# Kernel optimization log

Hardware: AMD Instinct MI355X
Metric: run time of the kernel (lower is better)

The kernel has to match this reference:

```python
import jax, jax.numpy as jnp
import numpy as np

# dims: batch, d_features(m), n_subsets, sub_size(k=ceil(m/n)), heads, d_k, d_v, conv kernel, d_out
B, M, N, K, H, DK, DV, KER, D = 512, 4096, 64, 64, 8, 32, 4, 3, 4096
DOUT_PER = D // N  # d_out_per_subset = 64
EPS_LN = 1e-5      # torch nn.LayerNorm default eps


def setup_inputs() -> dict:
    key = jax.random.key(0)
    ks = jax.random.split(key, 8)
    s = 0.02  # xavier-like scale
    return {
        "features": jax.random.normal(ks[0], (B, M), dtype=jnp.float32),
        # per-head permutation of the m feature indices (f_shuffle(m, h, seeds))
        "shuffled_index": jnp.argsort(jax.random.uniform(ks[1], (H, M)), axis=1).astype(jnp.int32),
        "gamma": jnp.ones((M,), jnp.float32),
        "beta": jnp.zeros((M,), jnp.float32),
        "W_q": (jax.random.normal(ks[2], (H * DK, K)) * s).astype(jnp.float32),   # Linear(k, h*d_k)
        "W_k": (jax.random.normal(ks[3], (H, DK, K)) * s).astype(jnp.float32),    # grouped Conv1d(h, h*d_k, kernel=k, stride=k)
        "W_v1": (jax.random.normal(ks[4], (H, DV, KER)) * s).astype(jnp.float32), # grouped Conv1d(h, h*d_v, kernel)
        "W_v2": (jax.random.normal(ks[5], (H, DV)) * s).astype(jnp.float32),      # grouped Conv1d(h*d_v, h, 1)
        "W_fc": (jax.random.normal(ks[6], (DOUT_PER, H * K)) * s).astype(jnp.float32),
    }


def reference(features, shuffled_index, gamma, beta, W_q, W_k, W_v1, W_v2, W_fc):
    b = features.shape[0]
    # LayerNorm over m (query path only)
    mu = features.mean(-1, keepdims=True)
    var = ((features - mu) ** 2).mean(-1, keepdims=True)
    q_in = (features - mu) / jnp.sqrt(var + EPS_LN) * gamma + beta

    # shuffled gather: [b, H, M]  (k*n == m here so k_pad/q_pad are no-ops)
    sf = features[:, shuffled_index]

    # query: [b, n, k] -> Linear(k, h*d_k) -> [b, H, N, DK]
    q = jnp.einsum('bnk,ek->bne', q_in.reshape(b, N, K), W_q)
    q = q.reshape(b, N, H, DK).transpose(0, 2, 1, 3)

    # key: grouped conv kernel=stride=k == per-subset contraction -> [b, H, DK, N]
    kf = sf.reshape(b, H, N, K)
    key_ = jnp.einsum('bhnk,hdk->bhdn', kf, W_k)

    # value: [b, N, H, K], right-pad by KER-1, depthwise conv -> relu -> 1x1 conv -> +residual
    v = kf.transpose(0, 2, 1, 3)  # [b, N, H, K]
    vp = jnp.pad(v, ((0, 0), (0, 0), (0, 0), (0, KER - 1)))
    win = jnp.stack([vp[..., t:t + K] for t in range(KER)], axis=-1)  # [b,N,H,K,KER]
    v1 = jnp.einsum('bnhpt,hdt->bnhdp', win, W_v1)
    v2 = jnp.einsum('bnhdp,hd->bnhp', jax.nn.relu(v1), W_v2)
    v = (v2 + v).transpose(0, 2, 1, 3)  # [b, H, N, K]

    # scaled dot-product attention, temperature = sqrt(m)
    attn = jax.nn.softmax(jnp.einsum('bhqd,bhdk->bhqk', q, key_) / jnp.sqrt(jnp.float32(M)), axis=-1)
    out = jnp.einsum('bhqk,bhks->bhqs', attn, v)           # [b, H, N, K]
    out = out.transpose(0, 2, 1, 3).reshape(b, N, H * K)   # [b, N, H*K]
    out = jnp.einsum('bnf,of->bno', out, W_fc).reshape(b, N * DOUT_PER)
    return out, attn.reshape(b * H, N, N)
```

## Files before the change

### kernel.cpp

```cpp
#include <hip/hip_runtime.h>

typedef __bf16 v8bf __attribute__((ext_vector_type(8)));
typedef __bf16 v4bf __attribute__((ext_vector_type(4)));
typedef __bf16 v2bf __attribute__((ext_vector_type(2)));
typedef float  v4f  __attribute__((ext_vector_type(4)));

namespace {

constexpr int kB = 512, kM = 4096, kH = 8;


__global__ __launch_bounds__(256) void k0_weights(
    const float* __restrict__ Wq, const float* __restrict__ Wk,
    const float* __restrict__ Wfc,
    __bf16* __restrict__ wq, __bf16* __restrict__ wk, __bf16* __restrict__ wfc) {
  int i = blockIdx.x * 256 + threadIdx.x;
  if (i < 16384) {
    int e = i >> 6, k = i & 63;
    int dst = ((e >> 4) * 2 + (k >> 5)) * 512 + (e & 15) * 32 + (k & 31);
    wq[dst] = (__bf16)(Wq[i] * 0.015625f);
  } else if (i < 32768) {
    int j = i - 16384;
    int e = j >> 6, k = j & 63;
    int dst = ((e >> 4) * 2 + (k >> 5)) * 512 + (e & 15) * 32 + (k & 31);
    wk[dst] = (__bf16)Wk[j];
  } else {
    int j = i - 32768;
    int o = j >> 9, f = j & 511;
    int dst = ((o >> 4) * 16 + (f >> 5)) * 512 + (o & 15) * 32 + (f & 31);
    wfc[dst] = (__bf16)Wfc[j];
  }
}

__global__ __launch_bounds__(256, 2) void k_fused(
    const float* __restrict__ feat, const int* __restrict__ sidx,
    const float* __restrict__ gamma, const float* __restrict__ beta,
    const __bf16* __restrict__ wq, const __bf16* __restrict__ wk,
    const float* __restrict__ Wv1, const float* __restrict__ Wv2,
    const __bf16* __restrict__ wfc, float* __restrict__ out) {
  __shared__ __align__(16) __bf16 smem[26624];
  __shared__ float red[4];
  __bf16* s_feat = smem;
  __bf16* s_qin  = smem + 4096;
  __bf16* s_kf   = smem + 8192;
  __bf16* s_q    = smem + 12800;
  __bf16* s_K    = smem + 15360;
  __bf16* s_vT   = smem + 17920;
  __bf16* s_o    = smem + 22528;
  __bf16* s_sc   = s_kf;

  const int b = blockIdx.x;
  const int t = threadIdx.x, w = t >> 6, lane = t & 63;
  const int quad = lane >> 4, l16 = lane & 15;

  const float4* frow4 = reinterpret_cast<const float4*>(feat + (size_t)b * kM);
  const float4* g4  = reinterpret_cast<const float4*>(gamma);
  const float4* be4 = reinterpret_cast<const float4*>(beta);
  float4 xs[4];
  float s = 0.f;
#pragma unroll
  for (int j = 0; j < 4; ++j) {
    xs[j] = frow4[t + j * 256];
    s += xs[j].x + xs[j].y + xs[j].z + xs[j].w;
  }
  int idxr[16], idxn[16];
#pragma unroll
  for (int j = 0; j < 16; ++j) idxr[j] = sidx[t + j * 256];
#pragma unroll
  for (int o = 32; o > 0; o >>= 1) s += __shfl_xor(s, o);
  if (lane == 0) red[w] = s;
  __syncthreads();
  const float mu = (red[0] + red[1] + red[2] + red[3]) * (1.f / kM);
  float var_p = 0.f;
#pragma unroll
  for (int j = 0; j < 4; ++j) {
    float d0 = xs[j].x - mu, d1 = xs[j].y - mu, d2 = xs[j].z - mu, d3 = xs[j].w - mu;
    var_p += d0 * d0 + d1 * d1 + d2 * d2 + d3 * d3;
  }
#pragma unroll
  for (int o = 32; o > 0; o >>= 1) var_p += __shfl_xor(var_p, o);
  __syncthreads();
  if (lane == 0) red[w] = var_p;
  __syncthreads();
  const float var  = (red[0] + red[1] + red[2] + red[3]) * (1.f / kM);
  const float rstd = rsqrtf(var + 1e-5f);
#pragma unroll
  for (int j = 0; j < 4; ++j) {
    const int i4 = t + j * 256;
    float4 g = g4[i4], bt = be4[i4];
    v4bf fb, qb;
    fb[0] = (__bf16)xs[j].x; fb[1] = (__bf16)xs[j].y;
    fb[2] = (__bf16)xs[j].z; fb[3] = (__bf16)xs[j].w;
    qb[0] = (__bf16)((xs[j].x - mu) * rstd * g.x + bt.x);
    qb[1] = (__bf16)((xs[j].y - mu) * rstd * g.y + bt.y);
    qb[2] = (__bf16)((xs[j].z - mu) * rstd * g.z + bt.z);
    qb[3] = (__bf16)((xs[j].w - mu) * rstd * g.w + bt.w);
    *(v4bf*)(s_feat + 4 * i4) = fb;
    const int n = (t >> 4) + 16 * j, k = 4 * (t & 15);
    const int dst = ((n >> 4) * 2 + (k >> 5)) * 512 + (n & 15) * 32 + (k & 31);
    *(v4bf*)(s_qin + dst) = qb;
  }
  if (t < 64) { v8bf z = {}; *(v8bf*)(s_kf + t * 72 + 64) = z; }
  __syncthreads();

  v4f acc[4] = {{0.f, 0.f, 0.f, 0.f}, {0.f, 0.f, 0.f, 0.f},
                {0.f, 0.f, 0.f, 0.f}, {0.f, 0.f, 0.f, 0.f}};

  for (int h = 0; h < kH; ++h) {
    {
      v4f dq0 = {0.f, 0.f, 0.f, 0.f}, dq1 = {0.f, 0.f, 0.f, 0.f};
#pragma unroll
      for (int kt = 0; kt < 2; ++kt) {
        v8bf a  = *(const v8bf*)(s_qin + (2 * w + kt) * 512 + l16 * 32 + 8 * quad);
        v8bf b0 = *(const v8bf*)(wq + (size_t)(4 * h + kt) * 512 + l16 * 32 + 8 * quad);
        v8bf b1 = *(const v8bf*)(wq + (size_t)(4 * h + 2 + kt) * 512 + l16 * 32 + 8 * quad);
        dq0 = __builtin_amdgcn_mfma_f32_16x16x32_bf16(a, b0, dq0, 0, 0, 0);
        dq1 = __builtin_amdgcn_mfma_f32_16x16x32_bf16(a, b1, dq1, 0, 0, 0);
      }
#pragma unroll
      for (int r = 0; r < 4; ++r) {
        s_q[(16 * w + 4 * quad + r) * 40 + l16]      = (__bf16)dq0[r];
        s_q[(16 * w + 4 * quad + r) * 40 + 16 + l16] = (__bf16)dq1[r];
      }
    }

    if (h < kH - 1) {
      const int* idxp = sidx + (h + 1) * kM;
#pragma unroll
      for (int j = 0; j < 16; ++j) idxn[j] = idxp[t + j * 256];
    }

#pragma unroll
    for (int j = 0; j < 16; ++j) {
      int i = t + j * 256;
      s_kf[(i >> 6) * 72 + (i & 63)] = s_feat[idxr[j]];
    }
    __syncthreads();

    {
      v4f dk0 = {0.f, 0.f, 0.f, 0.f}, dk1 = {0.f, 0.f, 0.f, 0.f};
#pragma unroll
      for (int kt = 0; kt < 2; ++kt) {
        v8bf a  = *(const v8bf*)(s_kf + (16 * w + l16) * 72 + 32 * kt + 8 * quad);
        v8bf b0 = *(const v8bf*)(wk + (size_t)(4 * h + kt) * 512 + l16 * 32 + 8 * quad);
        v8bf b1 = *(const v8bf*)(wk + (size_t)(4 * h + 2 + kt) * 512 + l16 * 32 + 8 * quad);
        dk0 = __builtin_amdgcn_mfma_f32_16x16x32_bf16(a, b0, dk0, 0, 0, 0);
        dk1 = __builtin_amdgcn_mfma_f32_16x16x32_bf16(a, b1, dk1, 0, 0, 0);
      }
#pragma unroll
      for (int r = 0; r < 4; ++r) {
        s_K[(16 * w + 4 * quad + r) * 40 + l16]      = (__bf16)dk0[r];
        s_K[(16 * w + 4 * quad + r) * 40 + 16 + l16] = (__bf16)dk1[r];
      }
    }

    {
      const int n = t & 63, p0 = (t >> 6) * 16;
      float w1[4][3], w2[4];
#pragma unroll
      for (int d = 0; d < 4; ++d) {
#pragma unroll
        for (int c = 0; c < 3; ++c) w1[d][c] = Wv1[(h * 4 + d) * 3 + c];
        w2[d] = Wv2[h * 4 + d];
      }
      v8bf xa = *(const v8bf*)(s_kf + n * 72 + p0);
      v8bf xb = *(const v8bf*)(s_kf + n * 72 + p0 + 8);
      v2bf xc = *(const v2bf*)(s_kf + n * 72 + p0 + 16);
      float x[18];
#pragma unroll
      for (int c = 0; c < 8; ++c) { x[c] = (float)xa[c]; x[c + 8] = (float)xb[c]; }
      x[16] = (float)xc[0]; x[17] = (float)xc[1];
#pragma unroll
      for (int pp = 0; pp < 16; ++pp) {
        float a0 = x[pp];
#pragma unroll
        for (int d = 0; d < 4; ++d) {
          float v1 = fmaf(x[pp + 2], w1[d][2], fmaf(x[pp + 1], w1[d][1], x[pp] * w1[d][0]));
          a0 = fmaf(fmaxf(v1, 0.f), w2[d], a0);
        }
        s_vT[(p0 + pp) * 72 + n] = (__bf16)a0;
      }
    }
    __syncthreads();

    {
      v4f ds[4] = {{0.f, 0.f, 0.f, 0.f}, {0.f, 0.f, 0.f, 0.f},
                   {0.f, 0.f, 0.f, 0.f}, {0.f, 0.f, 0.f, 0.f}};
      v8bf a = *(const v8bf*)(s_q + (16 * w + l16) * 40 + 8 * quad);
#pragma unroll
      for (int nt = 0; nt < 4; ++nt) {
        v8bf bb = *(const v8bf*)(s_K + (16 * nt + l16) * 40 + 8 * quad);
        ds[nt] = __builtin_amdgcn_mfma_f32_16x16x32_bf16(a, bb, ds[nt], 0, 0, 0);
      }
#pragma unroll
      for (int nt = 0; nt < 4; ++nt)
#pragma unroll
        for (int r = 0; r < 4; ++r)
          s_sc[(16 * w + 4 * quad + r) * 72 + 16 * nt + l16] = (__bf16)ds[nt][r];
    }

    float* attn_out = out + (size_t)kB * kM + ((size_t)(b * kH + h)) * 4096;
#pragma unroll
    for (int rr = 0; rr < 4; ++rr) {
      const int row = 16 * w + 4 * rr + quad;
      v4bf pv = *(const v4bf*)(s_sc + row * 72 + 4 * l16);
      float e0 = (float)pv[0], e1 = (float)pv[1], e2 = (float)pv[2], e3 = (float)pv[3];
      float mx = fmaxf(fmaxf(e0, e1), fmaxf(e2, e3));
#pragma unroll
      for (int mk = 8; mk > 0; mk >>= 1) mx = fmaxf(mx, __shfl_xor(mx, mk));
      e0 = __expf(e0 - mx); e1 = __expf(e1 - mx);
      e2 = __expf(e2 - mx); e3 = __expf(e3 - mx);
      float ssum = e0 + e1 + e2 + e3;
#pragma unroll
      for (int mk = 8; mk > 0; mk >>= 1) ssum += __shfl_xor(ssum, mk);
      const float inv = 1.0f / ssum;
      e0 *= inv; e1 *= inv; e2 *= inv; e3 *= inv;
      *(float4*)(attn_out + row * 64 + 4 * l16) = make_float4(e0, e1, e2, e3);
      v4bf st;
      st[0] = (__bf16)e0; st[1] = (__bf16)e1; st[2] = (__bf16)e2; st[3] = (__bf16)e3;
      *(v4bf*)(s_sc + row * 72 + 4 * l16) = st;
    }

    v4f dO[4] = {{0.f, 0.f, 0.f, 0.f}, {0.f, 0.f, 0.f, 0.f},
                 {0.f, 0.f, 0.f, 0.f}, {0.f, 0.f, 0.f, 0.f}};
#pragma unroll
    for (int kt = 0; kt < 2; ++kt) {
      v8bf a = *(const v8bf*)(s_sc + (16 * w + l16) * 72 + 32 * kt + 8 * quad);
#pragma unroll
      for (int st = 0; st < 4; ++st) {
        v8bf bb = *(const v8bf*)(s_vT + (16 * st + l16) * 72 + 32 * kt + 8 * quad);
        dO[st] = __builtin_amdgcn_mfma_f32_16x16x32_bf16(a, bb, dO[st], 0, 0, 0);
      }
    }

    {
      __bf16* ob = s_o + w * 1024;
#pragma unroll
      for (int st = 0; st < 4; ++st)
#pragma unroll
        for (int r = 0; r < 4; ++r)
          ob[(st >> 1) * 512 + (4 * quad + r) * 32 + (st & 1) * 16 + l16] = (__bf16)dO[st][r];
#pragma unroll
      for (int kt = 0; kt < 2; ++kt) {
        v8bf a = *(const v8bf*)(ob + kt * 512 + l16 * 32 + 8 * quad);
#pragma unroll
        for (int nt = 0; nt < 4; ++nt) {
          v8bf bb = *(const v8bf*)(wfc + (size_t)(nt * 16 + h * 2 + kt) * 512 + l16 * 32 + 8 * quad);
          acc[nt] = __builtin_amdgcn_mfma_f32_16x16x32_bf16(a, bb, acc[nt], 0, 0, 0);
        }
      }
    }
    __syncthreads();

    if (h < kH - 1) {
#pragma unroll
      for (int j = 0; j < 16; ++j) idxr[j] = idxn[j];
    }
  }

  float* orow = out + (size_t)b * kM;
#pragma unroll
  for (int nt = 0; nt < 4; ++nt)
#pragma unroll
    for (int r = 0; r < 4; ++r)
      orow[(16 * w + 4 * quad + r) * 64 + 16 * nt + l16] = acc[nt][r];
}

}

extern "C" void kernel_launch(void* const* d_in, const int* in_sizes, int n_in,
                              void* d_out, int out_size, void* d_ws, size_t ws_size,
                              hipStream_t stream) {
  (void)in_sizes; (void)n_in; (void)out_size; (void)ws_size;
  const float* features = (const float*)d_in[0];
  const int*   sidx     = (const int*)d_in[1];
  const float* gamma    = (const float*)d_in[2];
  const float* beta     = (const float*)d_in[3];
  const float* Wq       = (const float*)d_in[4];
  const float* Wk       = (const float*)d_in[5];
  const float* Wv1      = (const float*)d_in[6];
  const float* Wv2      = (const float*)d_in[7];
  const float* Wfc      = (const float*)d_in[8];
  float* out = (float*)d_out;

  char* ws = (char*)d_ws;
  __bf16* ws_wq  = (__bf16*)(ws);
  __bf16* ws_wk  = (__bf16*)(ws + 32768);
  __bf16* ws_wfc = (__bf16*)(ws + 65536);

  hipLaunchKernelGGL(k0_weights, dim3(256), dim3(256), 0, stream,
                     Wq, Wk, Wfc, ws_wq, ws_wk, ws_wfc);
  hipLaunchKernelGGL(k_fused, dim3(kB), dim3(256), 0, stream,
                     features, sidx, gamma, beta, ws_wq, ws_wk, Wv1, Wv2, ws_wfc, out);
}
```

Baseline: 137.3 us.

## Split heads across two 256-thread streams per block with smem reduction of outputs

Doubles the block to 512 threads, so two independent groups of four waves each process alternating heads (even and odd) using their own shared-memory buffers. This halves the serial per-block head loop and adds latency hiding within a block. The two partial fc accumulators are combined through shared memory at the end. Shared memory per block grows, and every __syncthreads now stalls both groups together, which may limit occupancy.

Measured after the change: 158.2 us. 1.15x slower.

```diff
diff --git a/kernel.cpp b/kernel.cpp
--- a/kernel.cpp
+++ b/kernel.cpp
@@ -32,48 +32,51 @@
   }
 }
 
-__global__ __launch_bounds__(256, 2) void k_fused(
+__global__ __launch_bounds__(512, 4) void k_fused(
     const float* __restrict__ feat, const int* __restrict__ sidx,
     const float* __restrict__ gamma, const float* __restrict__ beta,
     const __bf16* __restrict__ wq, const __bf16* __restrict__ wk,
     const float* __restrict__ Wv1, const float* __restrict__ Wv2,
     const __bf16* __restrict__ wfc, float* __restrict__ out) {
-  __shared__ __align__(16) __bf16 smem[26624];
-  __shared__ float red[4];
+  __shared__ __align__(16) __bf16 smem[36864];
+  __shared__ float red[8];
   __bf16* s_feat = smem;
   __bf16* s_qin  = smem + 4096;
-  __bf16* s_kf   = smem + 8192;
-  __bf16* s_q    = smem + 12800;
-  __bf16* s_K    = smem + 15360;
-  __bf16* s_vT   = smem + 17920;
-  __bf16* s_o    = smem + 22528;
+  __bf16* sb     = smem + 8192 + (threadIdx.x >> 8) * 14336;
+  __bf16* s_kf   = sb;
+  __bf16* s_q    = sb + 4608;
+  __bf16* s_K    = sb + 7168;
+  __bf16* s_vT   = sb + 9728;
   __bf16* s_sc   = s_kf;
 
   const int b = blockIdx.x;
-  const int t = threadIdx.x, w = t >> 6, lane = t & 63;
+  const int t = threadIdx.x;
+  const int stream = t >> 8, ts = t & 255;
+  const int w = t >> 6, w4 = w & 3, lane = t & 63;
   const int quad = lane >> 4, l16 = lane & 15;
 
   const float4* frow4 = reinterpret_cast<const float4*>(feat + (size_t)b * kM);
   const float4* g4  = reinterpret_cast<const float4*>(gamma);
   const float4* be4 = reinterpret_cast<const float4*>(beta);
-  float4 xs[4];
+  float4 xs[2];
   float s = 0.f;
 #pragma unroll
-  for (int j = 0; j < 4; ++j) {
-    xs[j] = frow4[t + j * 256];
+  for (int j = 0; j < 2; ++j) {
+    xs[j] = frow4[t + j * 512];
     s += xs[j].x + xs[j].y + xs[j].z + xs[j].w;
   }
   int idxr[16], idxn[16];
 #pragma unroll
-  for (int j = 0; j < 16; ++j) idxr[j] = sidx[t + j * 256];
+  for (int j = 0; j < 16; ++j) idxr[j] = sidx[stream * kM + ts + j * 256];
 #pragma unroll
   for (int o = 32; o > 0; o >>= 1) s += __shfl_xor(s, o);
   if (lane == 0) red[w] = s;
   __syncthreads();
-  const float mu = (red[0] + red[1] + red[2] + red[3]) * (1.f / kM);
+  const float mu = (red[0] + red[1] + red[2] + red[3] +
+                    red[4] + red[5] + red[6] + red[7]) * (1.f / kM);
   float var_p = 0.f;
 #pragma unroll
-  for (int j = 0; j < 4; ++j) {
+  for (int j = 0; j < 2; ++j) {
     float d0 = xs[j].x - mu, d1 = xs[j].y - mu, d2 = xs[j].z - mu, d3 = xs[j].w - mu;
     var_p += d0 * d0 + d1 * d1 + d2 * d2 + d3 * d3;
   }
@@ -82,11 +85,12 @@
   __syncthreads();
   if (lane == 0) red[w] = var_p;
   __syncthreads();
-  const float var  = (red[0] + red[1] + red[2] + red[3]) * (1.f / kM);
+  const float var  = (red[0] + red[1] + red[2] + red[3] +
+                      red[4] + red[5] + red[6] + red[7]) * (1.f / kM);
   const float rstd = rsqrtf(var + 1e-5f);
 #pragma unroll
-  for (int j = 0; j < 4; ++j) {
-    const int i4 = t + j * 256;
+  for (int j = 0; j < 2; ++j) {
+    const int i4 = t + j * 512;
     float4 g = g4[i4], bt = be4[i4];
     v4bf fb, qb;
     fb[0] = (__bf16)xs[j].x; fb[1] = (__bf16)xs[j].y;
@@ -96,22 +100,24 @@
     qb[2] = (__bf16)((xs[j].z - mu) * rstd * g.z + bt.z);
     qb[3] = (__bf16)((xs[j].w - mu) * rstd * g.w + bt.w);
     *(v4bf*)(s_feat + 4 * i4) = fb;
-    const int n = (t >> 4) + 16 * j, k = 4 * (t & 15);
+    const int n = i4 >> 4, k = 4 * (t & 15);
     const int dst = ((n >> 4) * 2 + (k >> 5)) * 512 + (n & 15) * 32 + (k & 31);
     *(v4bf*)(s_qin + dst) = qb;
   }
-  if (t < 64) { v8bf z = {}; *(v8bf*)(s_kf + t * 72 + 64) = z; }
+  if (ts < 64) { v8bf z = {}; *(v8bf*)(s_kf + ts * 72 + 64) = z; }
   __syncthreads();
 
   v4f acc[4] = {{0.f, 0.f, 0.f, 0.f}, {0.f, 0.f, 0.f, 0.f},
                 {0.f, 0.f, 0.f, 0.f}, {0.f, 0.f, 0.f, 0.f}};
 
-  for (int h = 0; h < kH; ++h) {
+  for (int it = 0; it < 4; ++it) {
+    const int h = 2 * it + stream;
+
     {
       v4f dq0 = {0.f, 0.f, 0.f, 0.f}, dq1 = {0.f, 0.f, 0.f, 0.f};
 #pragma unroll
       for (int kt = 0; kt < 2; ++kt) {
-        v8bf a  = *(const v8bf*)(s_qin + (2 * w + kt) * 512 + l16 * 32 + 8 * quad);
+        v8bf a  = *(const v8bf*)(s_qin + (2 * w4 + kt) * 512 + l16 * 32 + 8 * quad);
         v8bf b0 = *(const v8bf*)(wq + (size_t)(4 * h + kt) * 512 + l16 * 32 + 8 * quad);
         v8bf b1 = *(const v8bf*)(wq + (size_t)(4 * h + 2 + kt) * 512 + l16 * 32 + 8 * quad);
         dq0 = __builtin_amdgcn_mfma_f32_16x16x32_bf16(a, b0, dq0, 0, 0, 0);
@@ -119,20 +125,20 @@
       }
 #pragma unroll
       for (int r = 0; r < 4; ++r) {
-        s_q[(16 * w + 4 * quad + r) * 40 + l16]      = (__bf16)dq0[r];
-        s_q[(16 * w + 4 * quad + r) * 40 + 16 + l16] = (__bf16)dq1[r];
-      }
-    }
-
-    if (h < kH - 1) {
-      const int* idxp = sidx + (h + 1) * kM;
-#pragma unroll
-      for (int j = 0; j < 16; ++j) idxn[j] = idxp[t + j * 256];
+        s_q[(16 * w4 + 4 * quad + r) * 40 + l16]      = (__bf16)dq0[r];
+        s_q[(16 * w4 + 4 * quad + r) * 40 + 16 + l16] = (__bf16)dq1[r];
+      }
+    }
+
+    if (it < 3) {
+      const int* idxp = sidx + (size_t)(h + 2) * kM;
+#pragma unroll
+      for (int j = 0; j < 16; ++j) idxn[j] = idxp[ts + j * 256];
     }
 
 #pragma unroll
     for (int j = 0; j < 16; ++j) {
-      int i = t + j * 256;
+      int i = ts + j * 256;
       s_kf[(i >> 6) * 72 + (i & 63)] = s_feat[idxr[j]];
     }
     __syncthreads();
@@ -141,7 +147,7 @@
       v4f dk0 = {0.f, 0.f, 0.f, 0.f}, dk1 = {0.f, 0.f, 0.f, 0.f};
 #pragma unroll
       for (int kt = 0; kt < 2; ++kt) {
-        v8bf a  = *(const v8bf*)(s_kf + (16 * w + l16) * 72 + 32 * kt + 8 * quad);
+        v8bf a  = *(const v8bf*)(s_kf + (16 * w4 + l16) * 72 + 32 * kt + 8 * quad);
         v8bf b0 = *(const v8bf*)(wk + (size_t)(4 * h + kt) * 512 + l16 * 32 + 8 * quad);
         v8bf b1 = *(const v8bf*)(wk + (size_t)(4 * h + 2 + kt) * 512 + l16 * 32 + 8 * quad);
         dk0 = __builtin_amdgcn_mfma_f32_16x16x32_bf16(a, b0, dk0, 0, 0, 0);
@@ -149,13 +155,13 @@
       }
 #pragma unroll
       for (int r = 0; r < 4; ++r) {
-        s_K[(16 * w + 4 * quad + r) * 40 + l16]      = (__bf16)dk0[r];
-        s_K[(16 * w + 4 * quad + r) * 40 + 16 + l16] = (__bf16)dk1[r];
-      }
-    }
-
-    {
-      const int n = t & 63, p0 = (t >> 6) * 16;
+        s_K[(16 * w4 + 4 * quad + r) * 40 + l16]      = (__bf16)dk0[r];
+        s_K[(16 * w4 + 4 * quad + r) * 40 + 16 + l16] = (__bf16)dk1[r];
+      }
+    }
+
+    {
+      const int n = lane, p0 = w4 * 16;
       float w1[4][3], w2[4];
 #pragma unroll
       for (int d = 0; d < 4; ++d) {
@@ -186,7 +192,7 @@
     {
       v4f ds[4] = {{0.f, 0.f, 0.f, 0.f}, {0.f, 0.f, 0.f, 0.f},
                    {0.f, 0.f, 0.f, 0.f}, {0.f, 0.f, 0.f, 0.f}};
-      v8bf a = *(const v8bf*)(s_q + (16 * w + l16) * 40 + 8 * quad);
+      v8bf a = *(const v8bf*)(s_q + (16 * w4 + l16) * 40 + 8 * quad);
 #pragma unroll
       for (int nt = 0; nt < 4; ++nt) {
         v8bf bb = *(const v8bf*)(s_K + (16 * nt + l16) * 40 + 8 * quad);
@@ -196,13 +202,13 @@
       for (int nt = 0; nt < 4; ++nt)
 #pragma unroll
         for (int r = 0; r < 4; ++r)
-          s_sc[(16 * w + 4 * quad + r) * 72 + 16 * nt + l16] = (__bf16)ds[nt][r];
+          s_sc[(16 * w4 + 4 * quad + r) * 72 + 16 * nt + l16] = (__bf16)ds[nt][r];
     }
 
     float* attn_out = out + (size_t)kB * kM + ((size_t)(b * kH + h)) * 4096;
 #pragma unroll
     for (int rr = 0; rr < 4; ++rr) {
-      const int row = 16 * w + 4 * rr + quad;
+      const int row = 16 * w4 + 4 * rr + quad;
       v4bf pv = *(const v4bf*)(s_sc + row * 72 + 4 * l16);
       float e0 = (float)pv[0], e1 = (float)pv[1], e2 = (float)pv[2], e3 = (float)pv[3];
       float mx = fmaxf(fmaxf(e0, e1), fmaxf(e2, e3));
@@ -225,7 +231,7 @@
                  {0.f, 0.f, 0.f, 0.f}, {0.f, 0.f, 0.f, 0.f}};
 #pragma unroll
     for (int kt = 0; kt < 2; ++kt) {
-      v8bf a = *(const v8bf*)(s_sc + (16 * w + l16) * 72 + 32 * kt + 8 * quad);
+      v8bf a = *(const v8bf*)(s_sc + (16 * w4 + l16) * 72 + 32 * kt + 8 * quad);
 #pragma unroll
       for (int st = 0; st < 4; ++st) {
         v8bf bb = *(const v8bf*)(s_vT + (16 * st + l16) * 72 + 32 * kt + 8 * quad);
@@ -234,7 +240,7 @@
     }
 
     {
-      __bf16* ob = s_o + w * 1024;
+      __bf16* ob = s_kf + w4 * 1152;
 #pragma unroll
       for (int st = 0; st < 4; ++st)
 #pragma unroll
@@ -252,18 +258,31 @@
     }
     __syncthreads();
 
-    if (h < kH - 1) {
+    if (it < 3) {
 #pragma unroll
       for (int j = 0; j < 16; ++j) idxr[j] = idxn[j];
     }
   }
 
-  float* orow = out + (size_t)b * kM;
-#pragma unroll
-  for (int nt = 0; nt < 4; ++nt)
-#pragma unroll
-    for (int r = 0; r < 4; ++r)
-      orow[(16 * w + 4 * quad + r) * 64 + 16 * nt + l16] = acc[nt][r];
+  float* accf = (float*)smem;
+  if (stream == 0) {
+#pragma unroll
+    for (int nt = 0; nt < 4; ++nt)
+#pragma unroll
+      for (int r = 0; r < 4; ++r)
+        accf[(16 * w4 + 4 * quad + r) * 65 + 16 * nt + l16] = acc[nt][r];
+  }
+  __syncthreads();
+  if (stream == 1) {
+    float* orow = out + (size_t)b * kM;
+#pragma unroll
+    for (int nt = 0; nt < 4; ++nt)
+#pragma unroll
+      for (int r = 0; r < 4; ++r) {
+        const int row = 16 * w4 + 4 * quad + r, col = 16 * nt + l16;
+        orow[row * 64 + col] = acc[nt][r] + accf[row * 65 + col];
+      }
+  }
 }
 
 }
@@ -290,6 +309,6 @@
 
   hipLaunchKernelGGL(k0_weights, dim3(256), dim3(256), 0, stream,
                      Wq, Wk, Wfc, ws_wq, ws_wk, ws_wfc);
-  hipLaunchKernelGGL(k_fused, dim3(kB), dim3(256), 0, stream,
+  hipLaunchKernelGGL(k_fused, dim3(kB), dim3(512), 0, stream,
                      features, sidx, gamma, beta, ws_wq, ws_wk, Wv1, Wv2, ws_wfc, out);
 }
```

## Split heads across two blocks per batch row with atomic output accumulation

Applied to the files above, without the earlier changes.

The fused kernel now launches two blocks per batch row, each handling four of the eight heads, and accumulates the fc output into a pre-zeroed output buffer with atomicAdd. The weight-prep kernel is enlarged to also zero the output. Shared memory is reduced by reusing the kf buffer for the per-head attention output, and the launch bound is raised to allow three blocks per CU. This aims to fill the GPU better than 512 blocks did, in exchange for duplicated LayerNorm work per block, atomic traffic, and an extra output-zeroing pass.

After: 154.6 us. 12.7% more time.

```diff
diff --git a/kernel.cpp b/kernel.cpp
--- a/kernel.cpp
+++ b/kernel.cpp
@@ -13,8 +13,10 @@
 __global__ __launch_bounds__(256) void k0_weights(
     const float* __restrict__ Wq, const float* __restrict__ Wk,
     const float* __restrict__ Wfc,
-    __bf16* __restrict__ wq, __bf16* __restrict__ wk, __bf16* __restrict__ wfc) {
+    __bf16* __restrict__ wq, __bf16* __restrict__ wk, __bf16* __restrict__ wfc,
+    float* __restrict__ out) {
   int i = blockIdx.x * 256 + threadIdx.x;
+  reinterpret_cast<float4*>(out)[i] = make_float4(0.f, 0.f, 0.f, 0.f);
   if (i < 16384) {
     int e = i >> 6, k = i & 63;
     int dst = ((e >> 4) * 2 + (k >> 5)) * 512 + (e & 15) * 32 + (k & 31);
@@ -24,7 +26,7 @@
     int e = j >> 6, k = j & 63;
     int dst = ((e >> 4) * 2 + (k >> 5)) * 512 + (e & 15) * 32 + (k & 31);
     wk[dst] = (__bf16)Wk[j];
-  } else {
+  } else if (i < 65536) {
     int j = i - 32768;
     int o = j >> 9, f = j & 511;
     int dst = ((o >> 4) * 16 + (f >> 5)) * 512 + (o & 15) * 32 + (f & 31);
@@ -32,13 +34,13 @@
   }
 }
 
-__global__ __launch_bounds__(256, 2) void k_fused(
+__global__ __launch_bounds__(256, 3) void k_fused(
     const float* __restrict__ feat, const int* __restrict__ sidx,
     const float* __restrict__ gamma, const float* __restrict__ beta,
     const __bf16* __restrict__ wq, const __bf16* __restrict__ wk,
     const float* __restrict__ Wv1, const float* __restrict__ Wv2,
     const __bf16* __restrict__ wfc, float* __restrict__ out) {
-  __shared__ __align__(16) __bf16 smem[26624];
+  __shared__ __align__(16) __bf16 smem[22528];
   __shared__ float red[4];
   __bf16* s_feat = smem;
   __bf16* s_qin  = smem + 4096;
@@ -46,10 +48,9 @@
   __bf16* s_q    = smem + 12800;
   __bf16* s_K    = smem + 15360;
   __bf16* s_vT   = smem + 17920;
-  __bf16* s_o    = smem + 22528;
   __bf16* s_sc   = s_kf;
 
-  const int b = blockIdx.x;
+  const int b = blockIdx.x, half = blockIdx.y, h0 = 4 * half;
   const int t = threadIdx.x, w = t >> 6, lane = t & 63;
   const int quad = lane >> 4, l16 = lane & 15;
 
@@ -65,7 +66,7 @@
   }
   int idxr[16], idxn[16];
 #pragma unroll
-  for (int j = 0; j < 16; ++j) idxr[j] = sidx[t + j * 256];
+  for (int j = 0; j < 16; ++j) idxr[j] = sidx[(size_t)h0 * kM + t + j * 256];
 #pragma unroll
   for (int o = 32; o > 0; o >>= 1) s += __shfl_xor(s, o);
   if (lane == 0) red[w] = s;
@@ -96,17 +97,18 @@
     qb[2] = (__bf16)((xs[j].z - mu) * rstd * g.z + bt.z);
     qb[3] = (__bf16)((xs[j].w - mu) * rstd * g.w + bt.w);
     *(v4bf*)(s_feat + 4 * i4) = fb;
-    const int n = (t >> 4) + 16 * j, k = 4 * (t & 15);
+    const int n = i4 >> 4, k = 4 * (t & 15);
     const int dst = ((n >> 4) * 2 + (k >> 5)) * 512 + (n & 15) * 32 + (k & 31);
     *(v4bf*)(s_qin + dst) = qb;
   }
-  if (t < 64) { v8bf z = {}; *(v8bf*)(s_kf + t * 72 + 64) = z; }
   __syncthreads();
 
   v4f acc[4] = {{0.f, 0.f, 0.f, 0.f}, {0.f, 0.f, 0.f, 0.f},
                 {0.f, 0.f, 0.f, 0.f}, {0.f, 0.f, 0.f, 0.f}};
 
-  for (int h = 0; h < kH; ++h) {
+  for (int it = 0; it < 4; ++it) {
+    const int h = h0 + it;
+
     {
       v4f dq0 = {0.f, 0.f, 0.f, 0.f}, dq1 = {0.f, 0.f, 0.f, 0.f};
 #pragma unroll
@@ -124,8 +126,8 @@
       }
     }
 
-    if (h < kH - 1) {
-      const int* idxp = sidx + (h + 1) * kM;
+    if (it < 3) {
+      const int* idxp = sidx + (size_t)(h + 1) * kM;
 #pragma unroll
       for (int j = 0; j < 16; ++j) idxn[j] = idxp[t + j * 256];
     }
@@ -135,6 +137,7 @@
       int i = t + j * 256;
       s_kf[(i >> 6) * 72 + (i & 63)] = s_feat[idxr[j]];
     }
+    if (t < 64) { v8bf z = {}; *(v8bf*)(s_kf + t * 72 + 64) = z; }
     __syncthreads();
 
     {
@@ -155,7 +158,7 @@
     }
 
     {
-      const int n = t & 63, p0 = (t >> 6) * 16;
+      const int n = lane, p0 = w * 16;
       float w1[4][3], w2[4];
 #pragma unroll
       for (int d = 0; d < 4; ++d) {
@@ -234,7 +237,7 @@
     }
 
     {
-      __bf16* ob = s_o + w * 1024;
+      __bf16* ob = s_kf + w * 1152;
 #pragma unroll
       for (int st = 0; st < 4; ++st)
 #pragma unroll
@@ -252,7 +255,7 @@
     }
     __syncthreads();
 
-    if (h < kH - 1) {
+    if (it < 3) {
 #pragma unroll
       for (int j = 0; j < 16; ++j) idxr[j] = idxn[j];
     }
@@ -263,7 +266,7 @@
   for (int nt = 0; nt < 4; ++nt)
 #pragma unroll
     for (int r = 0; r < 4; ++r)
-      orow[(16 * w + 4 * quad + r) * 64 + 16 * nt + l16] = acc[nt][r];
+      atomicAdd(&orow[(16 * w + 4 * quad + r) * 64 + 16 * nt + l16], acc[nt][r]);
 }
 
 }
@@ -288,8 +291,8 @@
   __bf16* ws_wk  = (__bf16*)(ws + 32768);
   __bf16* ws_wfc = (__bf16*)(ws + 65536);
 
-  hipLaunchKernelGGL(k0_weights, dim3(256), dim3(256), 0, stream,
-                     Wq, Wk, Wfc, ws_wq, ws_wk, ws_wfc);
-  hipLaunchKernelGGL(k_fused, dim3(kB), dim3(256), 0, stream,
+  hipLaunchKernelGGL(k0_weights, dim3(2048), dim3(256), 0, stream,
+                     Wq, Wk, Wfc, ws_wq, ws_wk, ws_wfc, out);
+  hipLaunchKernelGGL(k_fused, dim3(kB, 2), dim3(256), 0, stream,
                      features, sidx, gamma, beta, ws_wq, ws_wk, Wv1, Wv2, ws_wfc, out);
 }
```
